# Optimization experiments

Hardware: AMD Instinct MI355X
Metric: run time of the kernel (lower is better)

The kernel has to match this reference:

```python
import math
import jax, jax.numpy as jnp
import numpy as np


def setup_inputs() -> dict:
    key = jax.random.key(0)
    ks = jax.random.split(key, 6)
    B, L, d_model = 8, 4096, 512
    s = 1.0 / math.sqrt(d_model)
    inp = {
        "x": jax.random.normal(ks[0], (B, L, d_model), dtype=jnp.float32),
        "Wq": jax.random.normal(ks[1], (d_model, d_model), dtype=jnp.float32) * s,
        "bq": jnp.zeros((d_model,), jnp.float32),
        "Wk": jax.random.normal(ks[2], (d_model, d_model), dtype=jnp.float32) * s,
        "bk": jnp.zeros((d_model,), jnp.float32),
        "Wv": jax.random.normal(ks[3], (d_model, d_model), dtype=jnp.float32) * s,
        "bv": jnp.zeros((d_model,), jnp.float32),
        "Wo": jax.random.normal(ks[4], (d_model, d_model), dtype=jnp.float32) * s,
        "bo": jnp.zeros((d_model,), jnp.float32),
    }
    return inp


N_HEADS = 8
FACTOR = 1


def reference(x, Wq, bq, Wk, bk, Wv, bv, Wo, bo):
    B, L, d_model = x.shape
    H = N_HEADS
    D = d_model // H
    # projections (torch Linear: x @ W.T + b), reshape to (B,H,L,D)
    def proj(W, b):
        y = jnp.einsum("bld,ed->ble", x, W) + b
        return y.reshape(B, L, H, D).transpose(0, 2, 1, 3)
    q = proj(Wq, bq)
    k = proj(Wk, bk)
    v = proj(Wv, bv)
    # FFT autocorrelation along time axis (axis=2)
    q_f = jnp.fft.rfft(q, axis=2)
    k_f = jnp.fft.rfft(k, axis=2)
    corr = jnp.fft.irfft(q_f * jnp.conj(k_f), n=L, axis=2)  # (B,H,L,D)
    k_top = max(1, int(FACTOR * math.log(L + 1)))
    k_top = min(k_top, L)
    corr_mean = corr.mean(axis=-1)  # (B,H,L)
    top_vals, top_idx = jax.lax.top_k(corr_mean, k_top)  # (B,H,k)
    weights = jax.nn.softmax(top_vals, axis=-1)  # (B,H,k)
    t = jnp.arange(L).reshape(1, 1, 1, L)
    idx = (t + top_idx[..., None]) % L  # (B,H,k,L)
    # gather rolled V per selected lag: (B,H,k,L,D)
    v_exp = jnp.broadcast_to(v[:, :, None], (B, H, k_top, L, D))
    gathered = jnp.take_along_axis(v_exp, idx[..., None], axis=3)
    out = jnp.einsum("bhkld,bhk->bhld", gathered, weights)
    out = out.transpose(0, 2, 1, 3).reshape(B, L, d_model)
    # dropout=0.0 (eval): identity
    return jnp.einsum("bld,ed->ble", out, Wo) + bo
```

## Files before the change

### kernel.cpp

```cpp
#include <hip/hip_runtime.h>
#include <cstdint>
#include <cstddef>

#define AS1 __attribute__((address_space(1)))
#define AS3 __attribute__((address_space(3)))

using half8  = __attribute__((ext_vector_type(8))) _Float16;
using half4v = __attribute__((ext_vector_type(4))) _Float16;
using half2v = __attribute__((ext_vector_type(2))) _Float16;
using f32x4  = __attribute__((ext_vector_type(4))) float;

__global__ void prep_all_kernel(const float* __restrict__ x,
                                const float* __restrict__ Wq, const float* __restrict__ Wk,
                                const float* __restrict__ Wv, const float* __restrict__ Wo,
                                const float* __restrict__ bq, const float* __restrict__ bk,
                                const float* __restrict__ bv,
                                _Float16* __restrict__ xh, _Float16* __restrict__ Bt,
                                _Float16* __restrict__ WoH,
                                float2* __restrict__ tw, float* __restrict__ bias) {
    const int bid = blockIdx.x;
    const int tid = threadIdx.x;
    if (bid < 16384) {
        int i = (bid * 256 + tid) * 4;
        float4 v = *(const float4*)(x + i);
        half4v h;
        h[0] = (_Float16)v.x; h[1] = (_Float16)v.y;
        h[2] = (_Float16)v.z; h[3] = (_Float16)v.w;
        *(half4v*)(xh + i) = h;
    } else if (bid < 19456) {
        int i = (bid - 16384) * 256 + tid;
        int e = i >> 9, k = i & 511;
        int proj = e >> 9, er = e & 511;
        const float* W = (proj == 0) ? Wq : ((proj == 1) ? Wk : Wv);
        Bt[i] = (_Float16)W[er * 512 + k];
    } else if (bid < 20480) {
        int i = (bid - 19456) * 256 + tid;
        WoH[i] = (_Float16)Wo[i];
    } else if (bid < 20496) {
        int p = (bid - 20480) * 256 + tid;
        double th = -2.0 * 3.14159265358979323846 * (double)p / 4096.0;
        tw[p] = make_float2((float)cos(th), (float)sin(th));
    } else {
        int i = (bid - 20496) * 256 + tid;
        bias[i] = (i < 512) ? bq[i] : ((i < 1024) ? bk[i - 512] : bv[i - 1024]);
    }
}

template <int MODE>
__global__ __launch_bounds__(256, 4) void gemm_f16_kernel(
    const _Float16* __restrict__ A, const _Float16* __restrict__ Bt,
    const float* __restrict__ bias,
    _Float16* __restrict__ qT, _Float16* __restrict__ kT,
    _Float16* __restrict__ vout, float* __restrict__ Cout)
{
    constexpr int NBLK  = (MODE == 0) ? 12 : 4;
    constexpr int PERXCD = (MODE == 0) ? 384 : 128;
    __shared__ _Float16 As[128 * 32];
    __shared__ _Float16 Bs[128 * 32];

    const int gi = (blockIdx.x & 7) * PERXCD + (blockIdx.x >> 3);
    const int mb = gi / NBLK;
    const int nb = gi - mb * NBLK;
    const int m0 = mb * 128, n0 = nb * 128;
    const int tid = threadIdx.x;
    const int wave = tid >> 6, lane = tid & 63;
    const int wm = (wave & 1) * 64, wn = (wave >> 1) * 64;
    const int lane15 = lane & 15, quad = lane >> 4;
    const int srow = lane >> 2;
    const int scolB = (lane & 3) * 16;

    f32x4 acc[4][4];
#pragma unroll
    for (int mi = 0; mi < 4; mi++)
#pragma unroll
        for (int ni = 0; ni < 4; ni++)
#pragma unroll
            for (int r = 0; r < 4; r++) acc[mi][ni][r] = 0.f;

    for (int kt = 0; kt < 16; kt++) {
        const int kg = kt * 32;
        __syncthreads();
#pragma unroll
        for (int i = 0; i < 2; i++) {
            const int rb = wave * 32 + i * 16;
            const char* ga = (const char*)A  + ((size_t)(m0 + rb + srow)) * 1024 + kg * 2 + scolB;
            const char* gb = (const char*)Bt + ((size_t)(n0 + rb + srow)) * 1024 + kg * 2 + scolB;
            __builtin_amdgcn_global_load_lds((const AS1 void*)ga, (AS3 void*)((char*)As + rb * 64), 16, 0, 0);
            __builtin_amdgcn_global_load_lds((const AS1 void*)gb, (AS3 void*)((char*)Bs + rb * 64), 16, 0, 0);
        }
        __syncthreads();
        half8 af[4], bfr[4];
#pragma unroll
        for (int mi = 0; mi < 4; mi++)
            af[mi] = *(const half8*)((const char*)As + (wm + mi * 16 + lane15) * 64 + quad * 16);
#pragma unroll
        for (int ni = 0; ni < 4; ni++)
            bfr[ni] = *(const half8*)((const char*)Bs + (wn + ni * 16 + lane15) * 64 + quad * 16);
#pragma unroll
        for (int mi = 0; mi < 4; mi++)
#pragma unroll
            for (int ni = 0; ni < 4; ni++)
                acc[mi][ni] = __builtin_amdgcn_mfma_f32_16x16x32_f16(af[mi], bfr[ni], acc[mi][ni], 0, 0, 0);
    }

    if (MODE == 1) {
#pragma unroll
        for (int mi = 0; mi < 4; mi++)
#pragma unroll
            for (int ni = 0; ni < 4; ni++) {
                const int n = n0 + wn + ni * 16 + lane15;
                const float bb = bias[n];
#pragma unroll
                for (int r = 0; r < 4; r++) {
                    const int m = m0 + wm + mi * 16 + quad * 4 + r;
                    Cout[(size_t)m * 512 + n] = acc[mi][ni][r] + bb;
                }
            }
        return;
    }
    const int proj = n0 >> 9;
    if (proj == 2) {
#pragma unroll
        for (int mi = 0; mi < 4; mi++)
#pragma unroll
            for (int ni = 0; ni < 4; ni++) {
                const int n = n0 + wn + ni * 16 + lane15;
                const int er = n - 1024, h = er >> 6, d = er & 63;
                const float bb = bias[n];
#pragma unroll
                for (int r = 0; r < 4; r++) {
                    const int m = m0 + wm + mi * 16 + quad * 4 + r;
                    const int b = m >> 12, l = m & 4095;
                    vout[((size_t)((b * 8 + h) * 4096 + l)) * 64 + d] = (_Float16)(acc[mi][ni][r] + bb);
                }
            }
        return;
    }
    _Float16* dst = (proj == 0) ? qT : kT;
    const int b = m0 >> 12;
    const int lbase = (m0 & 4095) + wm + quad * 4;
#pragma unroll
    for (int mi = 0; mi < 4; mi++)
#pragma unroll
        for (int ni = 0; ni < 4; ni++) {
            const int e = n0 + wn + ni * 16 + lane15;
            const int er = e & 511, h = er >> 6, d = er & 63;
            const float bb = bias[e];
            half4v o;
            o[0] = (_Float16)(acc[mi][ni][0] + bb);
            o[1] = (_Float16)(acc[mi][ni][1] + bb);
            o[2] = (_Float16)(acc[mi][ni][2] + bb);
            o[3] = (_Float16)(acc[mi][ni][3] + bb);
            *(half4v*)(dst + ((size_t)((b * 8 + h) * 64 + d)) * 4096 + lbase + mi * 16) = o;
        }
}

__device__ __forceinline__ float2 cmul(float2 a, float2 b) {
    return make_float2(a.x * b.x - a.y * b.y, a.x * b.y + a.y * b.x);
}
__device__ __forceinline__ float2 cmulc(float2 a, float cr, float ci) {
    return make_float2(a.x * cr - a.y * ci, a.x * ci + a.y * cr);
}
__device__ __forceinline__ int swz(int i) { return i ^ ((i >> 4) & 15); }

__device__ __forceinline__ void dft16(float2 x[16]) {
    constexpr float wc[10] = {1.f, 0.92387953f, 0.70710678f, 0.38268343f, 0.f,
                              0.f, -0.70710678f, 0.f, 0.f, -0.92387953f};
    constexpr float wsn[10] = {0.f, -0.38268343f, -0.70710678f, -0.92387953f, -1.f,
                               0.f, -0.70710678f, 0.f, 0.f, 0.38268343f};
    float2 t[16];
#pragma unroll
    for (int u = 0; u < 4; u++) {
        const float2 a = x[u], b = x[u + 4], c = x[u + 8], d = x[u + 12];
        const float2 Ea = make_float2(a.x + c.x, a.y + c.y);
        const float2 Oa = make_float2(a.x - c.x, a.y - c.y);
        const float2 Eb = make_float2(b.x + d.x, b.y + d.y);
        const float2 Ob = make_float2(b.x - d.x, b.y - d.y);
        const float2 y0 = make_float2(Ea.x + Eb.x, Ea.y + Eb.y);
        const float2 y1 = make_float2(Oa.x + Ob.y, Oa.y - Ob.x);
        const float2 y2 = make_float2(Ea.x - Eb.x, Ea.y - Eb.y);
        const float2 y3 = make_float2(Oa.x - Ob.y, Oa.y + Ob.x);
        t[4 * u + 0] = y0;
        t[4 * u + 1] = cmulc(y1, wc[u * 1], wsn[u * 1]);
        t[4 * u + 2] = cmulc(y2, wc[u * 2], wsn[u * 2]);
        t[4 * u + 3] = cmulc(y3, wc[u * 3], wsn[u * 3]);
    }
#pragma unroll
    for (int v = 0; v < 4; v++) {
        const float2 a = t[v], b = t[v + 4], c = t[v + 8], d = t[v + 12];
        const float2 Ea = make_float2(a.x + c.x, a.y + c.y);
        const float2 Oa = make_float2(a.x - c.x, a.y - c.y);
        const float2 Eb = make_float2(b.x + d.x, b.y + d.y);
        const float2 Ob = make_float2(b.x - d.x, b.y - d.y);
        x[v]      = make_float2(Ea.x + Eb.x, Ea.y + Eb.y);
        x[v + 4]  = make_float2(Oa.x + Ob.y, Oa.y - Ob.x);
        x[v + 8]  = make_float2(Ea.x - Eb.x, Ea.y - Eb.y);
        x[v + 12] = make_float2(Oa.x - Ob.y, Oa.y + Ob.x);
    }
}

__device__ __forceinline__ void fft4096_r16(float2* buf, const float2* __restrict__ tw,
                                            int tid) {
    float2 x[16];
    __syncthreads();
#pragma unroll
    for (int j = 0; j < 16; j++) x[j] = buf[swz(tid + 256 * j)];
    __syncthreads();
    dft16(x);
    buf[swz(16 * tid)] = x[0];
#pragma unroll
    for (int m = 1; m < 16; m++) buf[swz(16 * tid + m)] = cmul(x[m], tw[tid * m]);
    __syncthreads();
#pragma unroll
    for (int j = 0; j < 16; j++) x[j] = buf[swz(tid + 256 * j)];
    __syncthreads();
    dft16(x);
    {
        const int q = tid & 15, p = tid >> 4;
        const int base = q + 256 * p;
        buf[swz(base)] = x[0];
#pragma unroll
        for (int m = 1; m < 16; m++)
            buf[swz(base + 16 * m)] = cmul(x[m], tw[(p * m) << 4]);
    }
    __syncthreads();
#pragma unroll
    for (int j = 0; j < 16; j++) x[j] = buf[swz(tid + 256 * j)];
    __syncthreads();
    dft16(x);
#pragma unroll
    for (int m = 0; m < 16; m++) buf[swz(tid + 256 * m)] = x[m];
    __syncthreads();
}

__global__ __launch_bounds__(256) void fft_partial_kernel(
    const _Float16* __restrict__ qT, const _Float16* __restrict__ kT,
    const float2* __restrict__ tw, float2* __restrict__ spec)
{
    __shared__ float2 buf[4096];
    const int tid = threadIdx.x;
    const int bh = blockIdx.x >> 4, chunk = blockIdx.x & 15;
    float sx[16], sy[16];
#pragma unroll
    for (int i = 0; i < 16; i++) { sx[i] = 0.f; sy[i] = 0.f; }
    const _Float16* qb = qT + (size_t)bh * 64 * 4096;
    const _Float16* kb = kT + (size_t)bh * 64 * 4096;
    for (int dd = 0; dd < 4; dd++) {
        const int d = chunk * 4 + dd;
#pragma unroll
        for (int i = 0; i < 2; i++) {
            const int t0 = 2048 * i + tid * 8;
            const half8 fq = *(const half8*)(qb + d * 4096 + t0);
            const half8 fk = *(const half8*)(kb + d * 4096 + t0);
#pragma unroll
            for (int j = 0; j < 8; j++)
                buf[swz(t0 + j)] = make_float2((float)fq[j], (float)fk[j]);
        }
        fft4096_r16(buf, tw, tid);
#pragma unroll
        for (int i = 0; i < 16; i++) {
            const int f = tid + 256 * i;
            const float2 Zf = buf[swz(f)];
            const float2 Zm = buf[swz((4096 - f) & 4095)];
            const float Qr  = 0.5f * (Zf.x + Zm.x);
            const float Qi  = 0.5f * (Zf.y - Zm.y);
            const float cKr = 0.5f * (Zf.y + Zm.y);
            const float cKi = 0.5f * (Zf.x - Zm.x);
            sx[i] += Qr * cKr - Qi * cKi;
            sy[i] += Qr * cKi + Qi * cKr;
        }
        __syncthreads();
    }
    float2* out = spec + (size_t)blockIdx.x * 4096;
#pragma unroll
    for (int i = 0; i < 16; i++) out[tid + 256 * i] = make_float2(sx[i], sy[i]);
}

__global__ __launch_bounds__(256) void reduce_topk_kernel(
    const float2* __restrict__ spec, const float2* __restrict__ tw,
    int* __restrict__ top_idx, float* __restrict__ top_w)
{
    __shared__ float2 buf[4096];
    __shared__ float wv[4];
    __shared__ int wi[4];
    const int tid = threadIdx.x;
    const int bh = blockIdx.x;
#pragma unroll
    for (int i = 0; i < 16; i++) {
        const int f = tid + 256 * i;
        float sr = 0.f, si = 0.f;
        for (int c = 0; c < 16; c++) {
            const float2 v = spec[((size_t)(bh * 16 + c)) * 4096 + f];
            sr += v.x; si += v.y;
        }
        buf[swz(f)] = make_float2(sr, -si);
    }
    fft4096_r16(buf, tw, tid);
    float vals[8]; int idxs[8];
    for (int k = 0; k < 8; k++) {
        float best = -3.0e38f; int bi = 0;
#pragma unroll
        for (int i = 0; i < 16; i++) {
            const int f = tid + 256 * i;
            const float c = buf[swz(f)].x;
            if (c > best) { best = c; bi = f; }
        }
#pragma unroll
        for (int off = 32; off > 0; off >>= 1) {
            const float ov = __shfl_down(best, off);
            const int oi = __shfl_down(bi, off);
            if (ov > best || (ov == best && oi < bi)) { best = ov; bi = oi; }
        }
        if ((tid & 63) == 0) { wv[tid >> 6] = best; wi[tid >> 6] = bi; }
        __syncthreads();
        if (tid == 0) {
            best = wv[0]; bi = wi[0];
            for (int w = 1; w < 4; w++) {
                if (wv[w] > best || (wv[w] == best && wi[w] < bi)) { best = wv[w]; bi = wi[w]; }
            }
            vals[k] = best; idxs[k] = bi;
            buf[swz(bi)].x = -3.4e38f;
        }
        __syncthreads();
    }
    if (tid == 0) {
        const float scale = 1.f / (4096.f * 64.f);
        float e[8], s = 0.f;
        const float mx = vals[0] * scale;
        for (int k = 0; k < 8; k++) { e[k] = __expf(vals[k] * scale - mx); s += e[k]; }
        for (int k = 0; k < 8; k++) {
            top_w[bh * 8 + k] = e[k] / s;
            top_idx[bh * 8 + k] = idxs[k];
        }
    }
}

__global__ __launch_bounds__(256) void gather_kernel(
    const half2v* __restrict__ v2, const int* __restrict__ top_idx,
    const float* __restrict__ top_w, half2v* __restrict__ out2)
{
    const int seq = blockIdx.x;
    const int bh = seq >> 9;
    const int lgrp = seq & 511;
    const int b = bh >> 3, h = bh & 7;
    const int tid = threadIdx.x;
    const int l = lgrp * 8 + (tid >> 5);
    const int d2 = tid & 31;
    int idx[8]; float w[8];
#pragma unroll
    for (int k = 0; k < 8; k++) { idx[k] = top_idx[bh * 8 + k]; w[k] = top_w[bh * 8 + k]; }
    const half2v* vb = v2 + (size_t)bh * 4096 * 32;
    float a0 = 0.f, a1 = 0.f;
#pragma unroll
    for (int k = 0; k < 8; k++) {
        const int ls = (l + idx[k]) & 4095;
        const half2v pv = vb[ls * 32 + d2];
        a0 += w[k] * (float)pv[0];
        a1 += w[k] * (float)pv[1];
    }
    half2v o; o[0] = (_Float16)a0; o[1] = (_Float16)a1;
    out2[((size_t)(b * 4096 + l)) * 256 + h * 32 + d2] = o;
}

extern "C" void kernel_launch(void* const* d_in, const int* in_sizes, int n_in,
                              void* d_out, int out_size, void* d_ws, size_t ws_size,
                              hipStream_t stream) {
    (void)in_sizes; (void)n_in; (void)out_size; (void)ws_size;
    const float* x  = (const float*)d_in[0];
    const float* Wq = (const float*)d_in[1];
    const float* bq = (const float*)d_in[2];
    const float* Wk = (const float*)d_in[3];
    const float* bk = (const float*)d_in[4];
    const float* Wv = (const float*)d_in[5];
    const float* bv = (const float*)d_in[6];
    const float* Wo = (const float*)d_in[7];
    const float* bo = (const float*)d_in[8];
    float* out = (float*)d_out;

    char* ws = (char*)d_ws;
    size_t off = 0;
    auto alloc = [&](size_t bytes) -> void* {
        void* p = ws + off; off += (bytes + 255) & ~(size_t)255; return p;
    };
    _Float16* xh   = (_Float16*)alloc(33554432);
    _Float16* qT   = (_Float16*)alloc(33554432);
    _Float16* kT   = (_Float16*)alloc(33554432);
    _Float16* vbuf = (_Float16*)alloc(33554432);
    float2* spec   = (float2*)alloc(33554432);
    _Float16* BtH  = (_Float16*)alloc(1572864);
    _Float16* WoH  = (_Float16*)alloc(524288);
    float* biasQKV = (float*)alloc(6144);
    float2* tw     = (float2*)alloc(32768);
    int*   top_idx = (int*)alloc(2048);
    float* top_w   = (float*)alloc(2048);
    _Float16* out_pre = xh;

    prep_all_kernel<<<20502, 256, 0, stream>>>(x, Wq, Wk, Wv, Wo, bq, bk, bv,
                                               xh, BtH, WoH, tw, biasQKV);
    gemm_f16_kernel<0><<<3072, 256, 0, stream>>>(xh, BtH, biasQKV, qT, kT, vbuf, nullptr);
    fft_partial_kernel<<<1024, 256, 0, stream>>>(qT, kT, tw, spec);
    reduce_topk_kernel<<<64, 256, 0, stream>>>(spec, tw, top_idx, top_w);
    gather_kernel<<<32768, 256, 0, stream>>>((const half2v*)vbuf, top_idx, top_w,
                                             (half2v*)out_pre);
    gemm_f16_kernel<1><<<1024, 256, 0, stream>>>(out_pre, WoH, bo, nullptr, nullptr, nullptr, out);
}
```

Baseline: 366.6 us.

## Split spectrum reduction into parallel kernel, vectorize gather, reuse FFT registers

Moves the 16-chunk spectrum summation out of the 64-block top-k kernel into a separate 512-block kernel with float4 loads, so the reduction is no longer limited to 64 workgroups. The gather kernel now handles 8 halves per thread with 128-bit loads and stores, using a quarter as many blocks. The FFT helper returns its final values in registers so the partial kernel reads Zf from registers rather than shared memory. This adds one kernel launch and a small intermediate buffer.

New measurement: 333.0 us. 9.2% less time.

```diff
diff --git a/kernel.cpp b/kernel.cpp
--- a/kernel.cpp
+++ b/kernel.cpp
@@ -200,8 +200,7 @@
 }
 
 __device__ __forceinline__ void fft4096_r16(float2* buf, const float2* __restrict__ tw,
-                                            int tid) {
-    float2 x[16];
+                                            int tid, float2 (&x)[16]) {
     __syncthreads();
 #pragma unroll
     for (int j = 0; j < 16; j++) x[j] = buf[swz(tid + 256 * j)];
@@ -245,6 +244,7 @@
     for (int i = 0; i < 16; i++) { sx[i] = 0.f; sy[i] = 0.f; }
     const _Float16* qb = qT + (size_t)bh * 64 * 4096;
     const _Float16* kb = kT + (size_t)bh * 64 * 4096;
+    float2 x[16];
     for (int dd = 0; dd < 4; dd++) {
         const int d = chunk * 4 + dd;
 #pragma unroll
@@ -256,11 +256,11 @@
             for (int j = 0; j < 8; j++)
                 buf[swz(t0 + j)] = make_float2((float)fq[j], (float)fk[j]);
         }
-        fft4096_r16(buf, tw, tid);
+        fft4096_r16(buf, tw, tid, x);
 #pragma unroll
         for (int i = 0; i < 16; i++) {
             const int f = tid + 256 * i;
-            const float2 Zf = buf[swz(f)];
+            const float2 Zf = x[i];
             const float2 Zm = buf[swz((4096 - f) & 4095)];
             const float Qr  = 0.5f * (Zf.x + Zm.x);
             const float Qi  = 0.5f * (Zf.y - Zm.y);
@@ -276,8 +276,24 @@
     for (int i = 0; i < 16; i++) out[tid + 256 * i] = make_float2(sx[i], sy[i]);
 }
 
+__global__ __launch_bounds__(256) void sum_spec_kernel(
+    const float4* __restrict__ spec4, float4* __restrict__ ssum4)
+{
+    const int bh = blockIdx.x >> 3;
+    const int i4 = (blockIdx.x & 7) * 256 + threadIdx.x;
+    const float4* base = spec4 + (size_t)bh * 16 * 2048 + i4;
+    float4 s = make_float4(0.f, 0.f, 0.f, 0.f);
+#pragma unroll
+    for (int c = 0; c < 16; c++) {
+        const float4 v = base[(size_t)c * 2048];
+        s.x += v.x; s.y += v.y; s.z += v.z; s.w += v.w;
+    }
+    s.y = -s.y; s.w = -s.w;
+    ssum4[(size_t)bh * 2048 + i4] = s;
+}
+
 __global__ __launch_bounds__(256) void reduce_topk_kernel(
-    const float2* __restrict__ spec, const float2* __restrict__ tw,
+    const float2* __restrict__ ssum, const float2* __restrict__ tw,
     int* __restrict__ top_idx, float* __restrict__ top_w)
 {
     __shared__ float2 buf[4096];
@@ -288,14 +304,10 @@
 #pragma unroll
     for (int i = 0; i < 16; i++) {
         const int f = tid + 256 * i;
-        float sr = 0.f, si = 0.f;
-        for (int c = 0; c < 16; c++) {
-            const float2 v = spec[((size_t)(bh * 16 + c)) * 4096 + f];
-            sr += v.x; si += v.y;
-        }
-        buf[swz(f)] = make_float2(sr, -si);
-    }
-    fft4096_r16(buf, tw, tid);
+        buf[swz(f)] = ssum[(size_t)bh * 4096 + f];
+    }
+    float2 x[16];
+    fft4096_r16(buf, tw, tid, x);
     float vals[8]; int idxs[8];
     for (int k = 0; k < 8; k++) {
         float best = -3.0e38f; int bi = 0;
@@ -336,30 +348,34 @@
 }
 
 __global__ __launch_bounds__(256) void gather_kernel(
-    const half2v* __restrict__ v2, const int* __restrict__ top_idx,
-    const float* __restrict__ top_w, half2v* __restrict__ out2)
+    const half8* __restrict__ v8, const int* __restrict__ top_idx,
+    const float* __restrict__ top_w, half8* __restrict__ out8)
 {
     const int seq = blockIdx.x;
-    const int bh = seq >> 9;
-    const int lgrp = seq & 511;
+    const int bh = seq >> 7;
+    const int lgrp = seq & 127;
     const int b = bh >> 3, h = bh & 7;
     const int tid = threadIdx.x;
-    const int l = lgrp * 8 + (tid >> 5);
-    const int d2 = tid & 31;
+    const int l = lgrp * 32 + (tid >> 3);
+    const int d8 = tid & 7;
     int idx[8]; float w[8];
 #pragma unroll
     for (int k = 0; k < 8; k++) { idx[k] = top_idx[bh * 8 + k]; w[k] = top_w[bh * 8 + k]; }
-    const half2v* vb = v2 + (size_t)bh * 4096 * 32;
-    float a0 = 0.f, a1 = 0.f;
+    const half8* vb = v8 + (size_t)bh * 4096 * 8;
+    float a[8];
+#pragma unroll
+    for (int j = 0; j < 8; j++) a[j] = 0.f;
 #pragma unroll
     for (int k = 0; k < 8; k++) {
         const int ls = (l + idx[k]) & 4095;
-        const half2v pv = vb[ls * 32 + d2];
-        a0 += w[k] * (float)pv[0];
-        a1 += w[k] * (float)pv[1];
-    }
-    half2v o; o[0] = (_Float16)a0; o[1] = (_Float16)a1;
-    out2[((size_t)(b * 4096 + l)) * 256 + h * 32 + d2] = o;
+        const half8 pv = vb[(size_t)ls * 8 + d8];
+#pragma unroll
+        for (int j = 0; j < 8; j++) a[j] += w[k] * (float)pv[j];
+    }
+    half8 o;
+#pragma unroll
+    for (int j = 0; j < 8; j++) o[j] = (_Float16)a[j];
+    out8[((size_t)(b * 4096 + l)) * 64 + h * 8 + d8] = o;
 }
 
 extern "C" void kernel_launch(void* const* d_in, const int* in_sizes, int n_in,
@@ -387,6 +403,7 @@
     _Float16* kT   = (_Float16*)alloc(33554432);
     _Float16* vbuf = (_Float16*)alloc(33554432);
     float2* spec   = (float2*)alloc(33554432);
+    float2* ssum   = (float2*)alloc(2097152);
     _Float16* BtH  = (_Float16*)alloc(1572864);
     _Float16* WoH  = (_Float16*)alloc(524288);
     float* biasQKV = (float*)alloc(6144);
@@ -399,8 +416,9 @@
                                                xh, BtH, WoH, tw, biasQKV);
     gemm_f16_kernel<0><<<3072, 256, 0, stream>>>(xh, BtH, biasQKV, qT, kT, vbuf, nullptr);
     fft_partial_kernel<<<1024, 256, 0, stream>>>(qT, kT, tw, spec);
-    reduce_topk_kernel<<<64, 256, 0, stream>>>(spec, tw, top_idx, top_w);
-    gather_kernel<<<32768, 256, 0, stream>>>((const half2v*)vbuf, top_idx, top_w,
-                                             (half2v*)out_pre);
+    sum_spec_kernel<<<512, 256, 0, stream>>>((const float4*)spec, (float4*)ssum);
+    reduce_topk_kernel<<<64, 256, 0, stream>>>(ssum, tw, top_idx, top_w);
+    gather_kernel<<<8192, 256, 0, stream>>>((const half8*)vbuf, top_idx, top_w,
+                                            (half8*)out_pre);
     gemm_f16_kernel<1><<<1024, 256, 0, stream>>>(out_pre, WoH, bo, nullptr, nullptr, nullptr, out);
 }
```
